# Kernel tuning notes

Hardware: AMD Instinct MI355X
Metric: run time of the kernel (lower is better)

Reference implementation:

```python
import jax, jax.numpy as jnp
import numpy as np

B, E, F, Q = 16, 2048, 8192, 20
D, WD = 256, 300
NUM_ENTITY, NUM_WORD, NUM_RELATION = 100000, 50000, 600
NUM_LAYER = 3
PAGERANK_LAMBDA = 0.8
FACT_SCALE = 3.0
VERY_NEG = -100000000000.0
VERY_SMALL = 1e-10


def setup_inputs() -> dict:
    key = jax.random.key(0)
    ks = jax.random.split(key, 40)
    s = 0.05
    L = NUM_LAYER
    inp = {
        'local_entity': jax.random.randint(ks[0], (B, E), 0, NUM_ENTITY),
        'q2e_adj_mat': jax.random.uniform(ks[1], (B, E, 1), jnp.float32),
        'kb_fact_rel': jax.random.randint(ks[2], (B, F), 0, NUM_RELATION),
        'query_text': jax.random.randint(ks[3], (B, Q), 0, NUM_WORD),
        'answer_dist': jax.random.uniform(ks[4], (B, E), jnp.float32),
        'e2f_ent': jax.random.randint(ks[5], (B, F), 0, E),
        'f2e_ent': jax.random.randint(ks[6], (B, F), 0, E),
        'word_emb': jax.random.normal(ks[7], (NUM_WORD + 1, WD)) * s,
        'entity_emb': jax.random.normal(ks[8], (NUM_ENTITY + 1, WD)) * s,
        'relation_emb': jax.random.normal(ks[9], (NUM_RELATION + 1, 2 * WD)) * s,
        'entity_lin_w': jax.random.normal(ks[10], (D, WD)) * s,
        'entity_lin_b': jnp.zeros((D,)),
        'relation_lin_w': jax.random.normal(ks[11], (D, 2 * WD)) * s,
        'relation_lin_b': jnp.zeros((D,)),
        'lstm_w_ih': jax.random.normal(ks[12], (4 * D, WD)) * s,
        'lstm_w_hh': jax.random.normal(ks[13], (4 * D, D)) * s,
        'lstm_b_ih': jnp.zeros((4 * D,)),
        'lstm_b_hh': jnp.zeros((4 * D,)),
        'q2e_w': jax.random.normal(ks[14], (L, D, D)) * s,
        'q2e_b': jnp.zeros((L, D)),
        'e2q_w': jax.random.normal(ks[15], (L, D, 3 * D)) * s,
        'e2q_b': jnp.zeros((L, D)),
        'e2e_w': jax.random.normal(ks[16], (L, D, 3 * D)) * s,
        'e2e_b': jnp.zeros((L, D)),
        'kb_head_w': jax.random.normal(ks[17], (L, D, D)) * s,
        'kb_head_b': jnp.zeros((L, D)),
        'kb_tail_w': jax.random.normal(ks[18], (L, D, D)) * s,
        'kb_tail_b': jnp.zeros((L, D)),
        'kb_self_w': jax.random.normal(ks[19], (L, D, D)) * s,
        'kb_self_b': jnp.zeros((L, D)),
        'score_w': jax.random.normal(ks[20], (1, D)) * s,
        'score_b': jnp.zeros((1,)),
    }
    return inp


def _lstm(x, w_ih, w_hh, b_ih, b_hh):
    # torch LSTM, single layer, unidirectional, zero init state; gates (i,f,g,o)
    gx = jnp.einsum('btd,gd->btg', x, w_ih) + b_ih + b_hh  # [B,T,4H]
    H = w_hh.shape[1]
    init = (jnp.zeros((x.shape[0], H), x.dtype), jnp.zeros((x.shape[0], H), x.dtype))
    def step(carry, g):
        h, c = carry
        z = g + h @ w_hh.T
        i, f, gg, o = jnp.split(z, 4, axis=-1)
        c = jax.nn.sigmoid(f) * c + jax.nn.sigmoid(i) * jnp.tanh(gg)
        h = jax.nn.sigmoid(o) * jnp.tanh(c)
        return (h, c), h
    (h, _), hs = jax.lax.scan(step, init, jnp.swapaxes(gx, 0, 1))
    return jnp.swapaxes(hs, 0, 1), h  # [B,T,H], [B,H]


def _forward(local_entity, q2e_adj_mat, kb_fact_rel, query_text, e2f_ent, f2e_ent,
             word_emb, entity_emb, relation_emb,
             entity_lin_w, entity_lin_b, relation_lin_w, relation_lin_b,
             lstm_w_ih, lstm_w_hh, lstm_b_ih, lstm_b_hh,
             q2e_w, q2e_b, e2q_w, e2q_b, e2e_w, e2e_b,
             kb_head_w, kb_head_b, kb_tail_w, kb_tail_b, kb_self_w, kb_self_b,
             score_w, score_b):
    bidx = jnp.arange(B)[:, None]
    ent_mask = (local_entity != NUM_ENTITY).astype(jnp.float32)  # [B,E]
    q_mask = (query_text != NUM_WORD).astype(jnp.float32)        # [B,Q]

    # query LSTM encoding (dropout = identity in eval)
    qh, qlast = _lstm(word_emb[query_text], lstm_w_ih, lstm_w_hh, lstm_b_ih, lstm_b_hh)
    query_node = qlast[:, None, :]                               # [B,1,D]

    # fact embeddings
    lf = relation_emb[kb_fact_rel] @ relation_lin_w.T + relation_lin_b  # [B,F,D]
    div = jnp.sqrt(jnp.float32(D))

    # fact <-> query attention
    sim = jnp.einsum('bqd,bfd->bqf', qh, lf) / div
    sim = jax.nn.softmax(sim + (1.0 - q_mask)[:, :, None] * VERY_NEG, axis=1)
    att = jnp.einsum('bqf,bqd->bfd', sim, qh)
    Wf = jnp.sum(att * lf, axis=2) / div                          # [B,F]
    W_tilde = jnp.exp(Wf - jnp.max(Wf, axis=1, keepdims=True))    # [B,F]

    # e2f softmax normalizer: scatter-add fact weights onto head entities
    e2f_softmax = jnp.zeros((B, E), W_tilde.dtype).at[bidx, e2f_ent].add(W_tilde)
    e2f_softmax = jnp.maximum(e2f_softmax, VERY_SMALL)

    # entity embeddings (word_dim != entity_dim -> linear projection)
    le = entity_emb[local_entity] @ entity_lin_w.T + entity_lin_b  # [B,E,D]
    pagerank = q2e_adj_mat[..., 0]                                 # [B,E]

    for i in range(NUM_LAYER):
        q2e = jnp.broadcast_to(query_node @ q2e_w[i].T + q2e_b[i], (B, E, D))
        # fact update: self + gathered head-entity messages
        fact_self = lf @ kb_self_w[i].T + kb_self_b[i]
        head = le @ kb_head_w[i].T + kb_head_b[i]
        e2f_emb = jax.nn.relu(fact_self + jnp.take_along_axis(head, e2f_ent[:, :, None], axis=1))
        norm = W_tilde * jnp.take_along_axis(pagerank / e2f_softmax, e2f_ent, axis=1)  # [B,F]
        e2f_emb = e2f_emb * norm[:, :, None]
        # entity update: self + scattered tail messages
        tail = e2f_emb @ kb_tail_w[i].T + kb_tail_b[i]
        ent_self = le @ kb_self_w[i].T + kb_self_b[i]
        f2e_emb = jax.nn.relu(ent_self + jnp.zeros((B, E, D), le.dtype).at[bidx, f2e_ent].add(tail))
        pagerank = (PAGERANK_LAMBDA * jnp.zeros((B, E), norm.dtype).at[bidx, f2e_ent].add(norm)
                    + (1.0 - PAGERANK_LAMBDA) * pagerank)
        nxt = jnp.concatenate([le, q2e, FACT_SCALE * f2e_emb], axis=2)  # [B,E,3D]
        query_node = jnp.einsum('be,bed->bd', pagerank, nxt @ e2q_w[i].T + e2q_b[i])[:, None, :]
        le = jax.nn.relu(nxt @ e2e_w[i].T + e2e_b[i])

    score = (le @ score_w.T + score_b)[..., 0]                     # [B,E]
    return score


def reference(local_entity, q2e_adj_mat, kb_fact_rel, query_text, answer_dist,
              e2f_ent, f2e_ent, word_emb, entity_emb, relation_emb,
              entity_lin_w, entity_lin_b, relation_lin_w, relation_lin_b,
              lstm_w_ih, lstm_w_hh, lstm_b_ih, lstm_b_hh,
              q2e_w, q2e_b, e2q_w, e2q_b, e2e_w, e2e_b,
              kb_head_w, kb_head_b, kb_tail_w, kb_tail_b, kb_self_w, kb_self_b,
              score_w, score_b):
    return _forward(local_entity, q2e_adj_mat, kb_fact_rel, query_text, e2f_ent, f2e_ent,
                    word_emb, entity_emb, relation_emb,
                    entity_lin_w, entity_lin_b, relation_lin_w, relation_lin_b,
                    lstm_w_ih, lstm_w_hh, lstm_b_ih, lstm_b_hh,
                    q2e_w, q2e_b, e2q_w, e2q_b, e2e_w, e2e_b,
                    kb_head_w, kb_head_b, kb_tail_w, kb_tail_b, kb_self_w, kb_self_b,
                    score_w, score_b)
```

## Files before the change

kernel.cpp:

```cpp
#include <hip/hip_runtime.h>
#include <hip/hip_bf16.h>

typedef __hip_bfloat16 bf16;
typedef __attribute__((ext_vector_type(8))) short bf16x8;
typedef __attribute__((ext_vector_type(4))) float f32x4;

#define BB 16
#define EE 2048
#define FF 8192
#define QQ 20
#define DD 256
#define WDIM 300
#define NWORD 50000
#define VERY_NEG_F (-1.0e11f)

static __device__ __forceinline__ float b2f(bf16 x){ return __bfloat162float(x); }
static __device__ __forceinline__ bf16 f2b(float x){ return __float2bfloat16(x); }
static __device__ __forceinline__ float sigm(float x){ return 1.f/(1.f+expf(-x)); }
static __device__ __forceinline__ void ld4bf(const bf16* p, float v[4]){
  short4 s = *(const short4*)p;
  v[0]=b2f(*(const bf16*)&s.x); v[1]=b2f(*(const bf16*)&s.y);
  v[2]=b2f(*(const bf16*)&s.z); v[3]=b2f(*(const bf16*)&s.w);
}
static __device__ __forceinline__ void st4bf(bf16* p, float a,float b,float c,float d){
  unsigned short u[4]; bf16 t;
  t=f2b(a);u[0]=*(unsigned short*)&t; t=f2b(b);u[1]=*(unsigned short*)&t;
  t=f2b(c);u[2]=*(unsigned short*)&t; t=f2b(d);u[3]=*(unsigned short*)&t;
  *(short4*)p=*(short4*)u;
}

#define O_GX       0UL
#define O_QH       1310720UL
#define O_QNODE    1638400UL
#define O_RELLIN   1654784UL
#define O_WR       2270208UL
#define O_WMAX     2308864UL
#define O_WT       2309120UL
#define O_E2FS     2833408UL
#define O_PR       2964480UL
#define O_PRAGG    3095552UL
#define O_Q2EV     3226624UL
#define O_Q2EVB    3243008UL
#define O_RELSELF  3251200UL
#define O_NORM     3866624UL
#define O_WNXT     4390912UL
#define O_PRSUM    4440064UL
#define O_CNT      4440320UL
#define O_CUR      4571392UL
#define O_BSTART   4702464UL
#define O_BIDX     4834048UL
#define O_ELWPAD   5358336UL
#define O_FLAG     5522176UL
#define O_CVT      5522432UL
#define O_AGG      10915584UL
#define O_ENTSELF  27692800UL
#define O_LEA      44470016UL
#define O_LEB      61247232UL
#define O_HEAD     78024448UL
#define O_F2EEMB   94801664UL

#define C_ELB   0
#define C_RLW   256
#define C_RLB   153856
#define C_WIH   154112
#define C_WHH   461312
#define C_BIH   723456
#define C_BHH   724480
#define C_Q2EW  725504
#define C_Q2EB  922112
#define C_E2QW  922880
#define C_E2QB  1512704
#define C_E2EW  1513472
#define C_E2EB  2103296
#define C_KHW   2104064
#define C_KHB   2300672
#define C_KTW   2301440
#define C_KTB   2498048
#define C_KSW   2498816
#define C_KSB   2695424
#define C_SCW   2696192
#define C_SCB   2696448

__global__ __launch_bounds__(256) void k_sniff(const unsigned short* ee, int* flag){
  __shared__ int red[256];
  int c=0;
  for(int i=threadIdx.x;i<4096;i+=256){
    int ex=(ee[2*i]>>7)&0xFF;
    c += (ex>=192);
  }
  red[threadIdx.x]=c; __syncthreads();
  for(int o=128;o;o>>=1){ if(threadIdx.x<o) red[threadIdx.x]+=red[threadIdx.x+o]; __syncthreads(); }
  if(!threadIdx.x) flag[0] = (red[0]>64) ? 1 : 0;
}

struct CvtJobs{ const void* src[20]; bf16* dst[20]; int n[20]; int sc[20]; };
__global__ __launch_bounds__(256) void k_cvt(CvtJobs J, const int* dfl){
  const int isf=*dfl;
  int j=blockIdx.y;
  int n=J.n[j];
  int i4=(blockIdx.x*256+threadIdx.x)*4;
  if(i4>=n) return;
  float m = (J.sc[j] && ((i4%768)>=512)) ? 3.f : 1.f;
  bf16* d=J.dst[j]+i4;
  if(isf){
    const float* s=(const float*)J.src[j]+i4;
    if(i4+4<=n){ float4 t=*(const float4*)s; st4bf(d,t.x*m,t.y*m,t.z*m,t.w*m); }
    else for(int r=0;i4+r<n;r++) d[r]=f2b(s[r]*m);
  } else {
    const bf16* s=(const bf16*)J.src[j]+i4;
    if(i4+4<=n){ float v[4]; ld4bf(s,v); st4bf(d,v[0]*m,v[1]*m,v[2]*m,v[3]*m); }
    else for(int r=0;i4+r<n;r++) d[r]=f2b(b2f(s[r])*m);
  }
}

__global__ __launch_bounds__(256) void k_cvtwhh(const void* src, bf16* wf, const int* dfl){
  const int isf=*dfl;
  int fid=blockIdx.x*256+threadIdx.x;
  int lane=fid&63, kt=(fid>>6)&7, gt=fid>>9;
  int l16=lane&15, q=lane>>4;
  long so=(long)(gt*16+l16)*256 + kt*32 + q*8;
  float v[8];
  if(isf){ const float* s=(const float*)src+so;
    #pragma unroll
    for(int j=0;j<8;j++) v[j]=s[j];
  } else { const bf16* s=(const bf16*)src+so; ld4bf(s,v); ld4bf(s+4,v+4); }
  bf16* d=wf+(long)fid*8;
  st4bf(d,v[0],v[1],v[2],v[3]); st4bf(d+4,v[4],v[5],v[6],v[7]);
}

__global__ __launch_bounds__(256) void k_cvtelw(const void* src, bf16* dst, const int* dfl){
  const int isf=*dfl;
  int r=blockIdx.x;
  for(int c=threadIdx.x;c<320;c+=256){
    float v=0.f;
    if(c<300) v = isf ? ((const float*)src)[r*300+c] : b2f(((const bf16*)src)[r*300+c]);
    dst[(long)r*320+c]=f2b(v);
  }
}

__global__ __launch_bounds__(128) void k_ga0(const int* idx, const void* emb, bf16* A0, const int* dfl){
  const int isf=*dfl;
  int row=blockIdx.x; int ent=idx[row]; int t=threadIdx.x;
  bf16* dst=A0+(long)row*320;
  if(t<75){
    float v[4];
    if(isf){ float4 x=*(const float4*)((const float*)emb+(long)ent*WDIM+t*4);
             v[0]=x.x;v[1]=x.y;v[2]=x.z;v[3]=x.w; }
    else ld4bf((const bf16*)emb+(long)ent*WDIM+t*4, v);
    st4bf(dst+t*4, v[0],v[1],v[2],v[3]);
  } else if(t<80){
    st4bf(dst+t*4, 0.f,0.f,0.f,0.f);
  }
}

__global__ __launch_bounds__(256) void k_cnt(const int* f2e, int* cnt){
  int i=blockIdx.x*256+threadIdx.x;
  atomicAdd(&cnt[((i>>13)<<11)+f2e[i]], 1);
}
__global__ __launch_bounds__(1024) void k_scan(const int* cnt, int* bstart){
  __shared__ int ps[1024];
  int t=threadIdx.x;
  int loc[32]; int s=0;
  #pragma unroll
  for(int j=0;j<32;j++){ loc[j]=s; s+=cnt[t*32+j]; }
  ps[t]=s; __syncthreads();
  for(int off=1;off<1024;off<<=1){
    int v=(t>=off)?ps[t-off]:0;
    __syncthreads(); ps[t]+=v; __syncthreads();
  }
  int base=(t? ps[t-1]:0);
  #pragma unroll
  for(int j=0;j<32;j++) bstart[t*32+j]=base+loc[j];
  if(t==1023) bstart[32768]=ps[1023];
}
__global__ __launch_bounds__(256) void k_fill(const int* f2e, const int* bstart, int* cur, int* bidx){
  int i=blockIdx.x*256+threadIdx.x;
  int key=((i>>13)<<11)+f2e[i];
  int pos=bstart[key]+atomicAdd(&cur[key],1);
  bidx[pos]=i;
}

__global__ __launch_bounds__(256) void k_gx(const int* qtext, const void* wemb,
    const bf16* wih, const bf16* bih, const bf16* bhh, float* gx, const int* dfl){
  const int isf=*dfl;
  int bt=blockIdx.x;
  __shared__ float xr[WDIM];
  int w=qtext[bt];
  for(int k4=threadIdx.x*4;k4<WDIM;k4+=1024){
    if(isf){ float4 t=*(const float4*)((const float*)wemb+(long)w*WDIM+k4);
             xr[k4]=t.x;xr[k4+1]=t.y;xr[k4+2]=t.z;xr[k4+3]=t.w; }
    else   { float v[4]; ld4bf((const bf16*)wemb+(long)w*WDIM+k4,v);
             xr[k4]=v[0];xr[k4+1]=v[1];xr[k4+2]=v[2];xr[k4+3]=v[3]; }
  }
  __syncthreads();
  #pragma unroll
  for(int s=0;s<4;s++){
    int g=threadIdx.x+256*s;
    float acc=b2f(bih[g])+b2f(bhh[g]);
    const bf16* wr=wih+(long)g*WDIM;
    for(int k4=0;k4<WDIM;k4+=4){
      float v[4]; ld4bf(wr+k4,v);
      acc+=v[0]*xr[k4]+v[1]*xr[k4+1]+v[2]*xr[k4+2]+v[3]*xr[k4+3];
    }
    gx[bt*1024+g]=acc;
  }
}

#define NLB 8
__global__ __launch_bounds__(512) void k_lstm4(const float* gx, const bf16* wf,
    float* qh, float* qnode, bf16* hbuf, int* lcnt){
  __shared__ bf16  hlds[16*264];
  __shared__ float zs[4*16*32];
  __shared__ bf16  hsl[512];
  const int k=blockIdx.x, tid=threadIdx.x;
  const int wv=tid>>6, lane=tid&63, q=lane>>4, l16=lane&15;
  const int gt=(wv>>1)*16 + k*2 + (wv&1);
  const int b=tid>>5, u=tid&31, gu=k*32+u;
  bf16x8 wreg[8];
  #pragma unroll
  for(int kt=0;kt<8;kt++)
    wreg[kt]=*(const bf16x8*)(wf + (((long)(gt*8+kt))*64 + lane)*8);
  float c=0.f;
  float gxr[4];
  #pragma unroll
  for(int g=0;g<4;g++) gxr[g]=gx[(b*QQ+0)*1024 + g*256 + gu];
  for(int t=0;t<QQ;t++){
    f32x4 acc=(f32x4){0.f,0.f,0.f,0.f};
    if(t){
      while(__hip_atomic_load(lcnt+(t-1), __ATOMIC_RELAXED, __HIP_MEMORY_SCOPE_AGENT) < NLB)
        __builtin_amdgcn_s_sleep(2);
      __builtin_amdgcn_fence(__ATOMIC_ACQUIRE, "agent");
      __builtin_amdgcn_sched_barrier(0);
      const bf16* hb = hbuf + (t&1)*4096;
      {
        int r=tid>>5, cc=(tid&31)*8;
        unsigned long long v0=__hip_atomic_load((const unsigned long long*)(hb + r*256 + cc),
                       __ATOMIC_RELAXED, __HIP_MEMORY_SCOPE_AGENT);
        unsigned long long v1=__hip_atomic_load((const unsigned long long*)(hb + r*256 + cc + 4),
                       __ATOMIC_RELAXED, __HIP_MEMORY_SCOPE_AGENT);
        *(unsigned long long*)&hlds[r*264 + cc] = v0;
        *(unsigned long long*)&hlds[r*264 + cc + 4] = v1;
      }
      __syncthreads();
      #pragma unroll
      for(int kt=0;kt<8;kt++){
        bf16x8 af=*(const bf16x8*)&hlds[l16*264 + kt*32 + q*8];
        acc=__builtin_amdgcn_mfma_f32_16x16x32_bf16(af,wreg[kt],acc,0,0,0);
      }
    }
    #pragma unroll
    for(int r=0;r<4;r++) zs[(wv>>1)*512 + (q*4+r)*32 + (wv&1)*16 + l16]=acc[r];
    __syncthreads();
    float zi=zs[0*512+b*32+u]+gxr[0];
    float zf=zs[1*512+b*32+u]+gxr[1];
    float zg=zs[2*512+b*32+u]+gxr[2];
    float zo=zs[3*512+b*32+u]+gxr[3];
    {
      int tn=(t<QQ-1)?t+1:t;
      #pragma unroll
      for(int g=0;g<4;g++) gxr[g]=gx[(b*QQ+tn)*1024 + g*256 + gu];
    }
    c=sigm(zf)*c+sigm(zi)*tanhf(zg);
    float hv=sigm(zo)*tanhf(c);
    hsl[tid]=f2b(hv);
    __syncthreads();
    if(t<QQ-1){
      if(tid<128){
        bf16* hw=hbuf + ((t+1)&1)*4096;
        int bb=tid>>3, p=tid&7;
        unsigned long long v=*(unsigned long long*)&hsl[bb*32+p*4];
        __hip_atomic_store((unsigned long long*)(hw + bb*256 + k*32 + p*4), v,
                           __ATOMIC_RELAXED, __HIP_MEMORY_SCOPE_AGENT);
      }
      __syncthreads();
      if(tid==0)
        __hip_atomic_fetch_add(lcnt+t, 1, __ATOMIC_RELEASE, __HIP_MEMORY_SCOPE_AGENT);
    }
    __builtin_nontemporal_store(hv, &qh[(long)(b*QQ+t)*256+gu]);
    if(t==QQ-1) qnode[(b<<8)+gu]=hv;
  }
}

__global__ __launch_bounds__(256) void k_rel_lin(const void* remb, const bf16* rlw,
    const bf16* rlb, float* rel_lin, const int* dfl){
  const int isf=*dfl;
  int r=blockIdx.x;
  __shared__ float rr[2*WDIM];
  for(int k4=threadIdx.x*4;k4<2*WDIM;k4+=1024){
    if(isf){ float4 t=*(const float4*)((const float*)remb+(long)r*2*WDIM+k4);
             rr[k4]=t.x;rr[k4+1]=t.y;rr[k4+2]=t.z;rr[k4+3]=t.w; }
    else   { float v[4]; ld4bf((const bf16*)remb+(long)r*2*WDIM+k4,v);
             rr[k4]=v[0];rr[k4+1]=v[1];rr[k4+2]=v[2];rr[k4+3]=v[3]; }
  }
  __syncthreads();
  int d=threadIdx.x;
  float acc=b2f(rlb[d]);
  const bf16* wr=rlw+(long)d*2*WDIM;
  for(int k4=0;k4<2*WDIM;k4+=4){
    float v[4]; ld4bf(wr+k4,v);
    acc+=v[0]*rr[k4]+v[1]*rr[k4+1]+v[2]*rr[k4+2]+v[3]*rr[k4+3];
  }
  rel_lin[r*DD+d]=acc;
}

__global__ __launch_bounds__(256) void k_simwr(const float* qh, const float* rel_lin,
    const int* qtext, float* Wr){
  int b = blockIdx.x, rc = blockIdx.y;
  __shared__ float qhb[QQ*DD];
  __shared__ float qm[QQ];
  for(int i=threadIdx.x;i<QQ*DD;i+=256) qhb[i]=qh[b*QQ*DD+i];
  if(threadIdx.x<QQ) qm[threadIdx.x] = (qtext[b*QQ+threadIdx.x]!=NWORD)?0.f:VERY_NEG_F;
  __syncthreads();
  int r = rc*256+threadIdx.x;
  if(r>=601) return;
  float s[QQ];
  #pragma unroll
  for(int q=0;q<QQ;q++) s[q]=0.f;
  for(int k=0;k<DD;k++){
    float rl = rel_lin[r*DD+k];
    #pragma unroll
    for(int q=0;q<QQ;q++) s[q] += qhb[q*DD+k]*rl;
  }
  float m=-1e30f;
  #pragma unroll
  for(int q=0;q<QQ;q++){ s[q]*=0.0625f; m=fmaxf(m, s[q]+qm[q]); }
  float sum=0.f, w=0.f;
  #pragma unroll
  for(int q=0;q<QQ;q++){ float p=expf(s[q]+qm[q]-m); sum+=p; w+=p*s[q]; }
  Wr[b*601+r] = w/sum;
}

__global__ __launch_bounds__(256) void k_wmax(const float* Wr, const int* rel, float* wmax){
  int b=blockIdx.x; __shared__ float red[256];
  float m=-1e30f;
  for(int f=threadIdx.x;f<FF;f+=256) m=fmaxf(m, Wr[b*601+rel[b*FF+f]]);
  red[threadIdx.x]=m; __syncthreads();
  for(int o=128;o;o>>=1){ if(threadIdx.x<o) red[threadIdx.x]=fmaxf(red[threadIdx.x],red[threadIdx.x+o]); __syncthreads(); }
  if(!threadIdx.x) wmax[b]=red[0];
}
__global__ __launch_bounds__(256) void k_wt(const float* Wr, const int* rel,
    const float* wmax, const int* e2f, float* wt, float* e2fs){
  int i = blockIdx.x*256+threadIdx.x;
  int b = i>>13;
  float v = expf(Wr[b*601+rel[i]] - wmax[b]);
  wt[i]=v;
  atomicAdd(e2fs + (b<<11) + e2f[i], v);
}
__global__ __launch_bounds__(256) void k_prinit(const void* adj, float* pr, const int* dfl){
  const int isf=*dfl;
  int i4=(blockIdx.x*256+threadIdx.x)*4;
  if(isf){ *(float4*)(pr+i4)=*(const float4*)((const float*)adj+i4); }
  else { float v[4]; ld4bf((const bf16*)adj+i4,v);
         float4 t; t.x=v[0];t.y=v[1];t.z=v[2];t.w=v[3]; *(float4*)(pr+i4)=t; }
}

struct MG {
  const bf16* A; const bf16* W; const bf16* bias;
  bf16* out; int K;
  const bf16* Aq2; const bf16* Af2;
  const int* cnt; const bf16* addb;
  const bf16* W2; const bf16* bias2; bf16* out2;
};
template<int CONCAT,int EPI,int TK,int DUAL>
__global__ __launch_bounds__(256) void k_mgemm(MG p){
  const int m0 = blockIdx.x*64;
  const int wave = threadIdx.x>>6, lane = threadIdx.x&63;
  const int q = lane>>4, l16 = lane&15;
  const int n0 = wave*64;
  const int bidx_ = m0>>11;
  const bf16* Wp = p.W; const bf16* biasp = p.bias; bf16* outp = p.out;
  if(DUAL && blockIdx.y){ Wp=p.W2; biasp=p.bias2; outp=p.out2; }
  f32x4 acc[4][4];
  #pragma unroll
  for(int i=0;i<4;i++)
    #pragma unroll
    for(int j=0;j<4;j++) acc[i][j]=(f32x4){0.f,0.f,0.f,0.f};
  #pragma unroll
  for(int k0=0;k0<TK;k0+=32){
    int kk=k0+q*8;
    bf16x8 af[4], bw[4];
    #pragma unroll
    for(int mi=0;mi<4;mi++){
      int row=m0+mi*16+l16;
      const bf16* ap;
      if(CONCAT){
        if(kk<256)      ap=p.A  +(long)row*256+kk;
        else if(kk<512) ap=p.Aq2+(bidx_<<8)+(kk-256);
        else            ap=p.Af2+(long)row*256+(kk-512);
      } else ap=p.A+(long)row*TK+kk;
      af[mi]=*(const bf16x8*)ap;
    }
    #pragma unroll
    for(int ni=0;ni<4;ni++)
      bw[ni]=*(const bf16x8*)(Wp+(long)(n0+ni*16+l16)*TK+kk);
    #pragma unroll
    for(int mi=0;mi<4;mi++)
      #pragma unroll
      for(int ni=0;ni<4;ni++)
        acc[mi][ni]=__builtin_amdgcn_mfma_f32_16x16x32_bf16(af[mi],bw[ni],acc[mi][ni],0,0,0);
  }
  #pragma unroll
  for(int ni=0;ni<4;ni++){
    int col=n0+ni*16+l16;
    float bv=b2f(biasp[col]);
    #pragma unroll
    for(int mi=0;mi<4;mi++){
      #pragma unroll
      for(int r=0;r<4;r++){
        int row=m0+mi*16+q*4+r;
        float v=acc[mi][ni][r];
        if(EPI==0) v+=bv;
        else if(EPI==1) v=fmaxf(v+bv,0.f);
        else {
          v += (float)p.cnt[row]*bv + b2f(p.addb[(long)row*256+col]);
          v=fmaxf(v,0.f);
        }
        outp[(long)row*256+col]=f2b(v);
      }
    }
  }
}

__global__ __launch_bounds__(256) void k_small(const float* rel_lin, const bf16* selfw,
    const bf16* selfb, const float* qnode, const bf16* q2ew, const bf16* q2eb,
    float* relself, float* q2ev, bf16* q2evb){
  __shared__ float xr[DD];
  int d=threadIdx.x;
  if(blockIdx.x<601){
    int r=blockIdx.x;
    xr[d]=rel_lin[r*DD+d]; __syncthreads();
    float acc=b2f(selfb[d]);
    const bf16* wr=selfw+(long)d*DD;
    for(int k4=0;k4<DD;k4+=4){
      float v[4]; ld4bf(wr+k4,v);
      acc+=v[0]*xr[k4]+v[1]*xr[k4+1]+v[2]*xr[k4+2]+v[3]*xr[k4+3];
    }
    relself[r*DD+d]=acc;
  } else {
    int b=blockIdx.x-601;
    xr[d]=qnode[(b<<8)+d]; __syncthreads();
    float acc=b2f(q2eb[d]);
    const bf16* wr=q2ew+(long)d*DD;
    for(int k4=0;k4<DD;k4+=4){
      float v[4]; ld4bf(wr+k4,v);
      acc+=v[0]*xr[k4]+v[1]*xr[k4+1]+v[2]*xr[k4+2]+v[3]*xr[k4+3];
    }
    q2ev[(b<<8)+d]=acc;
    q2evb[(b<<8)+d]=f2b(acc);
  }
}

__global__ __launch_bounds__(256) void k_norm(const float* wt, const float* pr,
    const float* e2fs, const int* e2f, const int* f2e, float* normv, float* pragg){
  int i=blockIdx.x*256+threadIdx.x;
  int b=i>>13;
  int e=e2f[i];
  float v=wt[i]*pr[(b<<11)+e]/fmaxf(e2fs[(b<<11)+e],1e-10f);
  normv[i]=v;
  atomicAdd(pragg+(b<<11)+f2e[i], v);
}

__global__ __launch_bounds__(256) void k_agg(const int* bstart, const int* bidx,
    const int* rel, const int* e2f, const float* normv, const float* relself,
    const bf16* head, bf16* agg){
  int eidx=blockIdx.x*4+(threadIdx.x>>6);
  int lane=threadIdx.x&63;
  int b=eidx>>11;
  float a0=0.f,a1=0.f,a2=0.f,a3=0.f;
  int s=bstart[eidx], e=bstart[eidx+1];
  for(int i=s;i<e;i++){
    int f=bidx[i];
    int r=rel[f]; int ent=e2f[f]; float nv=normv[f];
    float4 rs=*(const float4*)&relself[r*DD+lane*4];
    float hd[4]; ld4bf(head+(long)(((b<<11)+ent)*DD+lane*4),hd);
    a0+=fmaxf(rs.x+hd[0],0.f)*nv; a1+=fmaxf(rs.y+hd[1],0.f)*nv;
    a2+=fmaxf(rs.z+hd[2],0.f)*nv; a3+=fmaxf(rs.w+hd[3],0.f)*nv;
  }
  st4bf(agg+(long)eidx*DD+lane*4, a0,a1,a2,a3);
}

__global__ __launch_bounds__(256) void k_wnxt(const float* pragg, float* pr, const bf16* le,
    const bf16* f2e, float* wnxt, float* prsum){
  __shared__ float r1[4*256];
  __shared__ float r3[4*256];
  __shared__ float rp[4];
  const int b=blockIdx.x, ch=blockIdx.y;
  const int wv=threadIdx.x>>6, lane=threadIdx.x&63;
  const int pe0=(b<<11)+ch*64+wv*16;
  float pv=0.f;
  if(lane<16){
    pv=0.8f*pragg[pe0+lane]+0.2f*pr[pe0+lane];
    pr[pe0+lane]=pv;
  }
  float a1[4]={0.f,0.f,0.f,0.f}, a3[4]={0.f,0.f,0.f,0.f}, ap=0.f;
  #pragma unroll
  for(int r=0;r<16;r++){
    float p=__shfl(pv, r, 64);
    long base=((long)(pe0+r))<<8;
    float v1[4],v3[4];
    ld4bf(le +base+lane*4, v1);
    ld4bf(f2e+base+lane*4, v3);
    #pragma unroll
    for(int j=0;j<4;j++){ a1[j]+=p*v1[j]; a3[j]+=p*v3[j]; }
    ap+=p;
  }
  #pragma unroll
  for(int j=0;j<4;j++){ r1[wv*256+lane*4+j]=a1[j]; r3[wv*256+lane*4+j]=a3[j]; }
  if(!lane) rp[wv]=ap;
  __syncthreads();
  const int t=threadIdx.x;
  float s1=r1[t]+r1[256+t]+r1[512+t]+r1[768+t];
  float s3=r3[t]+r3[256+t]+r3[512+t]+r3[768+t];
  atomicAdd(&wnxt[b*768+t], s1);
  atomicAdd(&wnxt[b*768+512+t], s3);
  if(!t) atomicAdd(&prsum[b], rp[0]+rp[1]+rp[2]+rp[3]);
}

__global__ __launch_bounds__(256) void k_qnode(const float* wnxt, const float* prsum,
    const float* q2ev, const bf16* w, const bf16* bias, float* qnode){
  int b=blockIdx.x, d=threadIdx.x;
  __shared__ float xr[768];
  float ps=prsum[b];
  xr[d]=wnxt[b*768+d];
  xr[256+d]=ps*q2ev[(b<<8)+d];
  xr[512+d]=wnxt[b*768+512+d];
  __syncthreads();
  float acc=0.f;
  const bf16* wr=w+(long)d*768;
  for(int k4=0;k4<768;k4+=4){
    float v[4]; ld4bf(wr+k4,v);
    acc+=v[0]*xr[k4]+v[1]*xr[k4+1]+v[2]*xr[k4+2]+v[3]*xr[k4+3];
  }
  qnode[(b<<8)+d]=acc+ps*b2f(bias[d]);
}

__global__ __launch_bounds__(256) void k_score(const bf16* le, const bf16* sw,
    const bf16* sb, void* out, const int* dfl){
  const int isf=*dfl;
  int o=blockIdx.x*4 + (threadIdx.x>>6);
  int lane=threadIdx.x&63;
  float v[4],wv[4];
  ld4bf(le+(long)o*DD+lane*4,v); ld4bf(sw+lane*4,wv);
  float acc=v[0]*wv[0]+v[1]*wv[1]+v[2]*wv[2]+v[3]*wv[3];
  for(int off=32;off;off>>=1) acc+=__shfl_down(acc,off,64);
  if(!lane){
    float r=acc+b2f(sb[0]);
    if(isf) ((float*)out)[o]=r; else ((bf16*)out)[o]=f2b(r);
  }
}

extern "C" void kernel_launch(void* const* d_in, const int* in_sizes, int n_in,
                              void* d_out, int out_size, void* d_ws, size_t ws_size,
                              hipStream_t stream){
  const int*  local_entity=(const int*)d_in[0];
  const void* q2e_adj     =d_in[1];
  const int*  kb_fact_rel =(const int*)d_in[2];
  const int*  query_text  =(const int*)d_in[3];
  const int*  e2f_ent     =(const int*)d_in[5];
  const int*  f2e_ent     =(const int*)d_in[6];
  const void* word_emb    =d_in[7];
  const void* entity_emb  =d_in[8];
  const void* relation_emb=d_in[9];

  char* ws=(char*)d_ws;
  float* gx      =(float*)(ws+O_GX);
  float* qh      =(float*)(ws+O_QH);
  float* qnode   =(float*)(ws+O_QNODE);
  float* rel_lin =(float*)(ws+O_RELLIN);
  float* Wr      =(float*)(ws+O_WR);
  float* wmax    =(float*)(ws+O_WMAX);
  float* wt      =(float*)(ws+O_WT);
  float* e2fs    =(float*)(ws+O_E2FS);
  float* pr      =(float*)(ws+O_PR);
  float* pragg   =(float*)(ws+O_PRAGG);
  float* q2ev    =(float*)(ws+O_Q2EV);
  bf16*  q2evb   =(bf16*)(ws+O_Q2EVB);
  float* relself =(float*)(ws+O_RELSELF);
  float* normv   =(float*)(ws+O_NORM);
  float* wnxt    =(float*)(ws+O_WNXT);
  float* prsum   =(float*)(ws+O_PRSUM);
  int*   cnt     =(int*)(ws+O_CNT);
  int*   cur     =(int*)(ws+O_CUR);
  int*   bstart  =(int*)(ws+O_BSTART);
  int*   bidx    =(int*)(ws+O_BIDX);
  bf16*  elwpad  =(bf16*)(ws+O_ELWPAD);
  int*   dflag   =(int*)(ws+O_FLAG);
  bf16*  cw      =(bf16*)(ws+O_CVT);
  bf16*  agg     =(bf16*)(ws+O_AGG);
  bf16*  A0      =(bf16*)(ws+O_AGG);
  bf16*  entself =(bf16*)(ws+O_ENTSELF);
  bf16*  leA     =(bf16*)(ws+O_LEA);
  bf16*  leB     =(bf16*)(ws+O_LEB);
  bf16*  headb   =(bf16*)(ws+O_HEAD);
  bf16*  f2eemb  =(bf16*)(ws+O_F2EEMB);
  bf16*  hbuf    =(bf16*)(ws+O_LEA);
  int*   lcnt    =(int*)(ws+O_LEA+16384);

  k_sniff<<<1,256,0,stream>>>((const unsigned short*)entity_emb, dflag);

  CvtJobs J;
  int cntj=0;
  auto add=[&](int in_idx, long coff, int n, int sc){
    J.src[cntj]=d_in[in_idx]; J.dst[cntj]=cw+coff; J.n[cntj]=n; J.sc[cntj]=sc; cntj++;
  };
  add(11,C_ELB,256,0);
  add(12,C_RLW,153600,0);  add(13,C_RLB,256,0);
  add(14,C_WIH,307200,0);
  add(16,C_BIH,1024,0);    add(17,C_BHH,1024,0);
  add(18,C_Q2EW,196608,0); add(19,C_Q2EB,768,0);
  add(20,C_E2QW,589824,1); add(21,C_E2QB,768,0);
  add(22,C_E2EW,589824,1); add(23,C_E2EB,768,0);
  add(24,C_KHW,196608,0);  add(25,C_KHB,768,0);
  add(26,C_KTW,196608,0);  add(27,C_KTB,768,0);
  add(28,C_KSW,196608,0);  add(29,C_KSB,768,0);
  add(30,C_SCW,256,0);     add(31,C_SCB,1,0);
  k_cvt<<<dim3(576,20),256,0,stream>>>(J, dflag);
  k_cvtwhh<<<128,256,0,stream>>>(d_in[15], cw+C_WHH, dflag);
  k_cvtelw<<<256,256,0,stream>>>(d_in[10], elwpad, dflag);

  hipMemsetAsync(cnt, 0, (size_t)2*BB*EE*4, stream);
  k_cnt <<<BB*FF/256,256,0,stream>>>(f2e_ent, cnt);
  k_scan<<<1,1024,0,stream>>>(cnt, bstart);
  k_fill<<<BB*FF/256,256,0,stream>>>(f2e_ent, bstart, cur, bidx);

  k_gx   <<<BB*QQ,256,0,stream>>>(query_text, word_emb, cw+C_WIH, cw+C_BIH, cw+C_BHH, gx, dflag);
  hipMemsetAsync(lcnt, 0, 128, stream);
  k_lstm4<<<NLB,512,0,stream>>>(gx, cw+C_WHH, qh, qnode, hbuf, lcnt);
  k_rel_lin<<<601,256,0,stream>>>(relation_emb, cw+C_RLW, cw+C_RLB, rel_lin, dflag);
  k_simwr<<<dim3(BB,3),256,0,stream>>>(qh, rel_lin, query_text, Wr);
  k_wmax <<<BB,256,0,stream>>>(Wr, kb_fact_rel, wmax);
  hipMemsetAsync(e2fs, 0, (size_t)BB*EE*4, stream);
  k_wt   <<<BB*FF/256,256,0,stream>>>(Wr, kb_fact_rel, wmax, e2f_ent, wt, e2fs);
  k_prinit<<<BB*EE/1024,256,0,stream>>>(q2e_adj, pr, dflag);

  k_ga0<<<BB*EE,128,0,stream>>>(local_entity, entity_emb, A0, dflag);
  {
    MG p{}; p.A=A0; p.W=elwpad; p.bias=cw+C_ELB; p.out=leA; p.K=320;
    k_mgemm<0,0,320,0><<<BB*EE/64,256,0,stream>>>(p);
  }

  bf16* le_cur=leA; bf16* le_nxt=leB;
  for(int i=0;i<3;i++){
    k_small<<<617,256,0,stream>>>(rel_lin, cw+C_KSW+(long)i*65536, cw+C_KSB+(long)i*256,
        qnode, cw+C_Q2EW+(long)i*65536, cw+C_Q2EB+(long)i*256, relself, q2ev, q2evb);
    {
      MG p{}; p.A=le_cur; p.K=256;
      p.W=cw+C_KHW+(long)i*65536;  p.bias=cw+C_KHB+(long)i*256;  p.out=headb;
      p.W2=cw+C_KSW+(long)i*65536; p.bias2=cw+C_KSB+(long)i*256; p.out2=entself;
      k_mgemm<0,0,256,1><<<dim3(BB*EE/64,2),256,0,stream>>>(p);
    }
    hipMemsetAsync(pragg, 0, (size_t)BB*EE*4, stream);
    k_norm<<<BB*FF/256,256,0,stream>>>(wt, pr, e2fs, e2f_ent, f2e_ent, normv, pragg);
    k_agg <<<BB*EE/4,256,0,stream>>>(bstart, bidx, kb_fact_rel, e2f_ent, normv, relself, headb, agg);
    {
      MG p{}; p.A=agg; p.W=cw+C_KTW+(long)i*65536; p.bias=cw+C_KTB+(long)i*256;
      p.out=f2eemb; p.K=256; p.cnt=cnt; p.addb=entself;
      k_mgemm<0,2,256,0><<<BB*EE/64,256,0,stream>>>(p);
    }
    hipMemsetAsync(wnxt, 0, (size_t)(BB*768*4+256), stream);
    k_wnxt <<<dim3(BB,32),256,0,stream>>>(pragg, pr, le_cur, f2eemb, wnxt, prsum);
    k_qnode<<<BB,256,0,stream>>>(wnxt, prsum, q2ev, cw+C_E2QW+(long)i*196608, cw+C_E2QB+(long)i*256, qnode);
    {
      MG p{}; p.A=le_cur; p.W=cw+C_E2EW+(long)i*196608; p.bias=cw+C_E2EB+(long)i*256;
      p.out=le_nxt; p.K=768; p.Aq2=q2evb; p.Af2=f2eemb;
      k_mgemm<1,1,768,0><<<BB*EE/64,256,0,stream>>>(p);
    }
    bf16* t=le_cur; le_cur=le_nxt; le_nxt=t;
  }

  k_score<<<BB*EE/4,256,0,stream>>>(le_cur, cw+C_SCW, cw+C_SCB, d_out, dflag);
}
```

Baseline: 1.118 ms.

## Fuse LSTM, relation linear, pagerank init and entity gather into one launch

Merges the serial 8-block LSTM kernel with three independent kernels: relation projection, pagerank init and entity-embedding gather. They become one launch, dispatched by block-index ranges. The goal is to hide the latency-bound recurrent LSTM loop behind the bandwidth-bound gather and projection work, and to drop several kernel launches. The LSTM step-completion counter increment is also weakened from a release to a relaxed atomic. That cuts fence cost but risks memory-ordering bugs, and the spinning LSTM blocks now compete with gather traffic for memory bandwidth.

```diff
diff --git a/kernel.cpp b/kernel.cpp
--- a/kernel.cpp
+++ b/kernel.cpp
@@ -138,21 +138,6 @@
   }
 }
 
-__global__ __launch_bounds__(128) void k_ga0(const int* idx, const void* emb, bf16* A0, const int* dfl){
-  const int isf=*dfl;
-  int row=blockIdx.x; int ent=idx[row]; int t=threadIdx.x;
-  bf16* dst=A0+(long)row*320;
-  if(t<75){
-    float v[4];
-    if(isf){ float4 x=*(const float4*)((const float*)emb+(long)ent*WDIM+t*4);
-             v[0]=x.x;v[1]=x.y;v[2]=x.z;v[3]=x.w; }
-    else ld4bf((const bf16*)emb+(long)ent*WDIM+t*4, v);
-    st4bf(dst+t*4, v[0],v[1],v[2],v[3]);
-  } else if(t<80){
-    st4bf(dst+t*4, 0.f,0.f,0.f,0.f);
-  }
-}
-
 __global__ __launch_bounds__(256) void k_cnt(const int* f2e, int* cnt){
   int i=blockIdx.x*256+threadIdx.x;
   atomicAdd(&cnt[((i>>13)<<11)+f2e[i]], 1);
@@ -207,100 +192,126 @@
 }
 
 #define NLB 8
-__global__ __launch_bounds__(512) void k_lstm4(const float* gx, const bf16* wf,
-    float* qh, float* qnode, bf16* hbuf, int* lcnt){
-  __shared__ bf16  hlds[16*264];
-  __shared__ float zs[4*16*32];
-  __shared__ bf16  hsl[512];
-  const int k=blockIdx.x, tid=threadIdx.x;
-  const int wv=tid>>6, lane=tid&63, q=lane>>4, l16=lane&15;
-  const int gt=(wv>>1)*16 + k*2 + (wv&1);
-  const int b=tid>>5, u=tid&31, gu=k*32+u;
-  bf16x8 wreg[8];
-  #pragma unroll
-  for(int kt=0;kt<8;kt++)
-    wreg[kt]=*(const bf16x8*)(wf + (((long)(gt*8+kt))*64 + lane)*8);
-  float c=0.f;
-  float gxr[4];
-  #pragma unroll
-  for(int g=0;g<4;g++) gxr[g]=gx[(b*QQ+0)*1024 + g*256 + gu];
-  for(int t=0;t<QQ;t++){
-    f32x4 acc=(f32x4){0.f,0.f,0.f,0.f};
-    if(t){
-      while(__hip_atomic_load(lcnt+(t-1), __ATOMIC_RELAXED, __HIP_MEMORY_SCOPE_AGENT) < NLB)
-        __builtin_amdgcn_s_sleep(2);
-      __builtin_amdgcn_fence(__ATOMIC_ACQUIRE, "agent");
-      __builtin_amdgcn_sched_barrier(0);
-      const bf16* hb = hbuf + (t&1)*4096;
-      {
-        int r=tid>>5, cc=(tid&31)*8;
-        unsigned long long v0=__hip_atomic_load((const unsigned long long*)(hb + r*256 + cc),
-                       __ATOMIC_RELAXED, __HIP_MEMORY_SCOPE_AGENT);
-        unsigned long long v1=__hip_atomic_load((const unsigned long long*)(hb + r*256 + cc + 4),
-                       __ATOMIC_RELAXED, __HIP_MEMORY_SCOPE_AGENT);
-        *(unsigned long long*)&hlds[r*264 + cc] = v0;
-        *(unsigned long long*)&hlds[r*264 + cc + 4] = v1;
+__global__ __launch_bounds__(512) void k_mega(const float* gx, const bf16* wf,
+    float* qh, float* qnode, bf16* hbuf, int* lcnt,
+    const void* remb, const bf16* rlw, const bf16* rlb, float* rel_lin,
+    const int* local_entity, const void* emb, bf16* A0,
+    const void* adj, float* pr, const int* dfl){
+  const int bid=blockIdx.x, tid=threadIdx.x;
+  if(bid<NLB){
+    __shared__ bf16  hlds[16*264];
+    __shared__ float zs[4*16*32];
+    __shared__ bf16  hsl[512];
+    const int k=bid;
+    const int wv=tid>>6, lane=tid&63, q=lane>>4, l16=lane&15;
+    const int gt=(wv>>1)*16 + k*2 + (wv&1);
+    const int b=tid>>5, u=tid&31, gu=k*32+u;
+    bf16x8 wreg[8];
+    #pragma unroll
+    for(int kt=0;kt<8;kt++)
+      wreg[kt]=*(const bf16x8*)(wf + (((long)(gt*8+kt))*64 + lane)*8);
+    float c=0.f;
+    float gxr[4];
+    #pragma unroll
+    for(int g=0;g<4;g++) gxr[g]=gx[(b*QQ+0)*1024 + g*256 + gu];
+    for(int t=0;t<QQ;t++){
+      f32x4 acc=(f32x4){0.f,0.f,0.f,0.f};
+      if(t){
+        while(__hip_atomic_load(lcnt+(t-1), __ATOMIC_RELAXED, __HIP_MEMORY_SCOPE_AGENT) < NLB)
+          __builtin_amdgcn_s_sleep(2);
+        __builtin_amdgcn_fence(__ATOMIC_ACQUIRE, "agent");
+        __builtin_amdgcn_sched_barrier(0);
+        const bf16* hb = hbuf + (t&1)*4096;
+        {
+          int r=tid>>5, cc=(tid&31)*8;
+          unsigned long long v0=__hip_atomic_load((const unsigned long long*)(hb + r*256 + cc),
+                         __ATOMIC_RELAXED, __HIP_MEMORY_SCOPE_AGENT);
+          unsigned long long v1=__hip_atomic_load((const unsigned long long*)(hb + r*256 + cc + 4),
+                         __ATOMIC_RELAXED, __HIP_MEMORY_SCOPE_AGENT);
+          *(unsigned long long*)&hlds[r*264 + cc] = v0;
+          *(unsigned long long*)&hlds[r*264 + cc + 4] = v1;
+        }
+        __syncthreads();
+        #pragma unroll
+        for(int kt=0;kt<8;kt++){
+          bf16x8 af=*(const bf16x8*)&hlds[l16*264 + kt*32 + q*8];
+          acc=__builtin_amdgcn_mfma_f32_16x16x32_bf16(af,wreg[kt],acc,0,0,0);
+        }
       }
+      #pragma unroll
+      for(int r=0;r<4;r++) zs[(wv>>1)*512 + (q*4+r)*32 + (wv&1)*16 + l16]=acc[r];
       __syncthreads();
-      #pragma unroll
-      for(int kt=0;kt<8;kt++){
-        bf16x8 af=*(const bf16x8*)&hlds[l16*264 + kt*32 + q*8];
-        acc=__builtin_amdgcn_mfma_f32_16x16x32_bf16(af,wreg[kt],acc,0,0,0);
+      float zi=zs[0*512+b*32+u]+gxr[0];
+      float zf=zs[1*512+b*32+u]+gxr[1];
+      float zg=zs[2*512+b*32+u]+gxr[2];
+      float zo=zs[3*512+b*32+u]+gxr[3];
+      { int tn=(t<QQ-1)?t+1:t;
+        #pragma unroll
+        for(int g=0;g<4;g++) gxr[g]=gx[(b*QQ+tn)*1024 + g*256 + gu];
       }
-    }
-    #pragma unroll
-    for(int r=0;r<4;r++) zs[(wv>>1)*512 + (q*4+r)*32 + (wv&1)*16 + l16]=acc[r];
+      c=sigm(zf)*c+sigm(zi)*tanhf(zg);
+      float hv=sigm(zo)*tanhf(c);
+      hsl[tid]=f2b(hv);
+      __syncthreads();
+      if(t<QQ-1){
+        if(tid<128){
+          bf16* hw=hbuf + ((t+1)&1)*4096;
+          int bb=tid>>3, p=tid&7;
+          unsigned long long v=*(unsigned long long*)&hsl[bb*32+p*4];
+          __hip_atomic_store((unsigned long long*)(hw + bb*256 + k*32 + p*4), v,
+                             __ATOMIC_RELAXED, __HIP_MEMORY_SCOPE_AGENT);
+        }
+        __syncthreads();
+        if(tid==0)
+          __hip_atomic_fetch_add(lcnt+t, 1, __ATOMIC_RELAXED, __HIP_MEMORY_SCOPE_AGENT);
+      }
+      __builtin_nontemporal_store(hv, &qh[(long)(b*QQ+t)*256+gu]);
+      if(t==QQ-1) qnode[(b<<8)+gu]=hv;
+    }
+  } else if(bid<309){
+    __shared__ float rr[2][2*WDIM];
+    const int isf=*dfl;
+    const int half=tid>>8, d=tid&255;
+    const int r=(bid-8)*2+half;
+    if(r<601){
+      for(int k4=d*4;k4<2*WDIM;k4+=1024){
+        if(isf){ float4 t4=*(const float4*)((const float*)remb+(long)r*2*WDIM+k4);
+                 rr[half][k4]=t4.x;rr[half][k4+1]=t4.y;rr[half][k4+2]=t4.z;rr[half][k4+3]=t4.w; }
+        else   { float v[4]; ld4bf((const bf16*)remb+(long)r*2*WDIM+k4,v);
+                 rr[half][k4]=v[0];rr[half][k4+1]=v[1];rr[half][k4+2]=v[2];rr[half][k4+3]=v[3]; }
+      }
+    }
     __syncthreads();
-    float zi=zs[0*512+b*32+u]+gxr[0];
-    float zf=zs[1*512+b*32+u]+gxr[1];
-    float zg=zs[2*512+b*32+u]+gxr[2];
-    float zo=zs[3*512+b*32+u]+gxr[3];
-    {
-      int tn=(t<QQ-1)?t+1:t;
-      #pragma unroll
-      for(int g=0;g<4;g++) gxr[g]=gx[(b*QQ+tn)*1024 + g*256 + gu];
-    }
-    c=sigm(zf)*c+sigm(zi)*tanhf(zg);
-    float hv=sigm(zo)*tanhf(c);
-    hsl[tid]=f2b(hv);
-    __syncthreads();
-    if(t<QQ-1){
-      if(tid<128){
-        bf16* hw=hbuf + ((t+1)&1)*4096;
-        int bb=tid>>3, p=tid&7;
-        unsigned long long v=*(unsigned long long*)&hsl[bb*32+p*4];
-        __hip_atomic_store((unsigned long long*)(hw + bb*256 + k*32 + p*4), v,
-                           __ATOMIC_RELAXED, __HIP_MEMORY_SCOPE_AGENT);
+    if(r<601){
+      float acc=b2f(rlb[d]);
+      const bf16* wr=rlw+(long)d*2*WDIM;
+      for(int k4=0;k4<2*WDIM;k4+=4){
+        float v[4]; ld4bf(wr+k4,v);
+        acc+=v[0]*rr[half][k4]+v[1]*rr[half][k4+1]+v[2]*rr[half][k4+2]+v[3]*rr[half][k4+3];
       }
-      __syncthreads();
-      if(tid==0)
-        __hip_atomic_fetch_add(lcnt+t, 1, __ATOMIC_RELEASE, __HIP_MEMORY_SCOPE_AGENT);
-    }
-    __builtin_nontemporal_store(hv, &qh[(long)(b*QQ+t)*256+gu]);
-    if(t==QQ-1) qnode[(b<<8)+gu]=hv;
-  }
-}
-
-__global__ __launch_bounds__(256) void k_rel_lin(const void* remb, const bf16* rlw,
-    const bf16* rlb, float* rel_lin, const int* dfl){
-  const int isf=*dfl;
-  int r=blockIdx.x;
-  __shared__ float rr[2*WDIM];
-  for(int k4=threadIdx.x*4;k4<2*WDIM;k4+=1024){
-    if(isf){ float4 t=*(const float4*)((const float*)remb+(long)r*2*WDIM+k4);
-             rr[k4]=t.x;rr[k4+1]=t.y;rr[k4+2]=t.z;rr[k4+3]=t.w; }
-    else   { float v[4]; ld4bf((const bf16*)remb+(long)r*2*WDIM+k4,v);
-             rr[k4]=v[0];rr[k4+1]=v[1];rr[k4+2]=v[2];rr[k4+3]=v[3]; }
-  }
-  __syncthreads();
-  int d=threadIdx.x;
-  float acc=b2f(rlb[d]);
-  const bf16* wr=rlw+(long)d*2*WDIM;
-  for(int k4=0;k4<2*WDIM;k4+=4){
-    float v[4]; ld4bf(wr+k4,v);
-    acc+=v[0]*rr[k4]+v[1]*rr[k4+1]+v[2]*rr[k4+2]+v[3]*rr[k4+3];
-  }
-  rel_lin[r*DD+d]=acc;
+      rel_lin[r*DD+d]=acc;
+    }
+  } else if(bid<325){
+    const int isf=*dfl;
+    int i4=((bid-309)*512+tid)*4;
+    if(isf){ *(float4*)(pr+i4)=*(const float4*)((const float*)adj+i4); }
+    else { float v[4]; ld4bf((const bf16*)adj+i4,v);
+           float4 t; t.x=v[0];t.y=v[1];t.z=v[2];t.w=v[3]; *(float4*)(pr+i4)=t; }
+  } else {
+    const int isf=*dfl;
+    int row=(bid-325)*4+(tid>>7); int t=tid&127;
+    int ent=local_entity[row];
+    bf16* dst=A0+(long)row*320;
+    if(t<75){
+      float v[4];
+      if(isf){ float4 x=*(const float4*)((const float*)emb+(long)ent*WDIM+t*4);
+               v[0]=x.x;v[1]=x.y;v[2]=x.z;v[3]=x.w; }
+      else ld4bf((const bf16*)emb+(long)ent*WDIM+t*4, v);
+      st4bf(dst+t*4, v[0],v[1],v[2],v[3]);
+    } else if(t<80){
+      st4bf(dst+t*4, 0.f,0.f,0.f,0.f);
+    }
+  }
 }
 
 __global__ __launch_bounds__(256) void k_simwr(const float* qh, const float* rel_lin,
@@ -345,13 +356,6 @@
   float v = expf(Wr[b*601+rel[i]] - wmax[b]);
   wt[i]=v;
   atomicAdd(e2fs + (b<<11) + e2f[i], v);
-}
-__global__ __launch_bounds__(256) void k_prinit(const void* adj, float* pr, const int* dfl){
-  const int isf=*dfl;
-  int i4=(blockIdx.x*256+threadIdx.x)*4;
-  if(isf){ *(float4*)(pr+i4)=*(const float4*)((const float*)adj+i4); }
-  else { float v[4]; ld4bf((const bf16*)adj+i4,v);
-         float4 t; t.x=v[0];t.y=v[1];t.z=v[2];t.w=v[3]; *(float4*)(pr+i4)=t; }
 }
 
 struct MG {
@@ -625,15 +629,15 @@
 
   k_gx   <<<BB*QQ,256,0,stream>>>(query_text, word_emb, cw+C_WIH, cw+C_BIH, cw+C_BHH, gx, dflag);
   hipMemsetAsync(lcnt, 0, 128, stream);
-  k_lstm4<<<NLB,512,0,stream>>>(gx, cw+C_WHH, qh, qnode, hbuf, lcnt);
-  k_rel_lin<<<601,256,0,stream>>>(relation_emb, cw+C_RLW, cw+C_RLB, rel_lin, dflag);
+  k_mega<<<8517,512,0,stream>>>(gx, cw+C_WHH, qh, qnode, hbuf, lcnt,
+      relation_emb, cw+C_RLW, cw+C_RLB, rel_lin,
+      local_entity, entity_emb, A0,
+      q2e_adj, pr, dflag);
   k_simwr<<<dim3(BB,3),256,0,stream>>>(qh, rel_lin, query_text, Wr);
   k_wmax <<<BB,256,0,stream>>>(Wr, kb_fact_rel, wmax);
   hipMemsetAsync(e2fs, 0, (size_t)BB*EE*4, stream);
   k_wt   <<<BB*FF/256,256,0,stream>>>(Wr, kb_fact_rel, wmax, e2f_ent, wt, e2fs);
-  k_prinit<<<BB*EE/1024,256,0,stream>>>(q2e_adj, pr, dflag);
-
-  k_ga0<<<BB*EE,128,0,stream>>>(local_entity, entity_emb, A0, dflag);
+
   {
     MG p{}; p.A=A0; p.W=elwpad; p.bias=cw+C_ELB; p.out=leA; p.K=320;
     k_mgemm<0,0,320,0><<<BB*EE/64,256,0,stream>>>(p);
```

Result: faster. 1.081 ms (-3.3%).
